# Kernel optimization log

Measured on AMD Instinct MI355X. Metric: run time of the kernel, lower is better.

## Reference

```python
import jax, jax.numpy as jnp
import numpy as np

N_NODES = 100000
N_EDGES = 3200000
ALPHA_KCL = 1.0
ALPHA_KVL = 1.0
EPS = 1e-6


def setup_inputs() -> dict:
    key = jax.random.key(0)
    k1, k2, k3, k4 = jax.random.split(key, 4)
    node_features = jax.random.normal(k1, (N_NODES, 4), dtype=jnp.float32)
    edge_index = jax.random.randint(k2, (2, N_EDGES), 0, N_NODES, dtype=jnp.int64)
    edge_logits = jax.random.normal(k3, (N_EDGES,), dtype=jnp.float32)
    edge_params = jax.random.uniform(k4, (N_EDGES, 2), dtype=jnp.float32)
    return {
        "node_features": node_features,
        "edge_index": edge_index,
        "edge_logits": edge_logits,
        "edge_params": edge_params,
    }


def reference(node_features, edge_index, edge_logits, edge_params):
    n_nodes = node_features.shape[0]
    edge_probs = jax.nn.sigmoid(edge_logits)  # [E]
    src = edge_index[0]  # [E]
    dst = edge_index[1]  # [E]
    v = node_features[:, 0]  # [N] voltage column
    # per-edge current: |v_src - v_dst| / (R + X + eps) * prob
    v_diff = jnp.abs(v[src] - v[dst])
    impedance = edge_params[:, 0] + edge_params[:, 1]
    current = v_diff / (impedance + EPS) * edge_probs  # [E]
    # KCL: each edge subtracts its current at src, adds at dst
    node_sum = (
        jax.ops.segment_sum(current, dst, num_segments=n_nodes)
        - jax.ops.segment_sum(current, src, num_segments=n_nodes)
    )  # [N]
    kcl_loss = jnp.mean(node_sum ** 2)
    # KVL (simplified): mean of per-column unbiased variance of edge_params
    kvl_loss = jnp.var(edge_params, axis=0, ddof=1).mean()
    return ALPHA_KCL * kcl_loss + ALPHA_KVL * kvl_loss
```

## Files before the change

kernel.cpp:

```cpp
#include <hip/hip_runtime.h>
#include <math.h>

#define N_NODES 100000
#define N_EDGES 3200000
#define EPS_F 1e-6f

#define SLICE_N 20000
#define NSLICE  5
#define NCHUNK  64
#define C_PAIRS (N_EDGES / 2 / NCHUNK)
#define SBATCH  8

#define NVARB   6250
#define NKCLB   391

#define PK_OFF    64
#define PART_OFF  (PK_OFF + 2 * N_EDGES)
#define VARP_OFF  (PART_OFF + NCHUNK * N_NODES)
#define KCLP_OFF  (VARP_OFF + 4 * NVARB)
#define WS_FLOATS (KCLP_OFF + NKCLB + 64)

__device__ __forceinline__ float wave_reduce(float v) {
    #pragma unroll
    for (int off = 32; off > 0; off >>= 1) v += __shfl_down(v, off, 64);
    return v;
}

__device__ __forceinline__ void fadd_agent(float* p, float v) {
    unsafeAtomicAdd(p, v);
}

__device__ __forceinline__ unsigned short f2bf(float f) {
    unsigned u = __float_as_uint(f);
    unsigned r = ((u >> 16) & 1u) + 0x7FFFu;
    return (unsigned short)((u + r) >> 16);
}
__device__ __forceinline__ float bf2f(unsigned short h) {
    return __uint_as_float(((unsigned)h) << 16);
}

__global__ __launch_bounds__(256) void prep_kernel(
    const float*  __restrict__ nf,
    const void*   __restrict__ eidx,
    const float*  __restrict__ logits,
    const float2* __restrict__ params,
    float*        __restrict__ ws)
{
    __shared__ float red[4][4];
    const int* i32 = (const int*)eidx;

    int any = 0;
    #pragma unroll
    for (int k = 1; k < 32; k += 2) any |= i32[k];
    const bool is32 = (any != 0);

    const int t = blockIdx.x * blockDim.x + threadIdx.x;

    int2 sp, dp;
    if (is32) {
        sp = ((const int2*)i32)[t];
        dp = ((const int2*)(i32 + N_EDGES))[t];
    } else {
        const int4 a = ((const int4*)i32)[t];
        const int4 b = ((const int4*)(i32 + 2 * N_EDGES))[t];
        sp = make_int2(a.x, a.z);
        dp = make_int2(b.x, b.z);
    }

    const float vs0 = nf[sp.x * 4];
    const float vd0 = nf[dp.x * 4];
    const float vs1 = nf[sp.y * 4];
    const float vd1 = nf[dp.y * 4];

    const float4 pp = ((const float4*)params)[t];
    const float2 lg = ((const float2*)logits)[t];
    const float w0 = (1.0f / (1.0f + __expf(-lg.x))) / (pp.x + pp.y + EPS_F);
    const float w1 = (1.0f / (1.0f + __expf(-lg.y))) / (pp.z + pp.w + EPS_F);
    const float c0 = fabsf(vs0 - vd0) * w0;
    const float c1 = fabsf(vs1 - vd1) * w1;

    int4 pk;
    pk.x = (int)((unsigned)sp.x | ((unsigned)dp.x << 17));
    pk.y = (int)((((unsigned)dp.x) >> 15) | ((unsigned)f2bf(c0) << 2));
    pk.z = (int)((unsigned)sp.y | ((unsigned)dp.y << 17));
    pk.w = (int)((((unsigned)dp.y) >> 15) | ((unsigned)f2bf(c1) << 2));
    ((int4*)(ws + PK_OFF))[t] = pk;

    float s0 = pp.x + pp.z;
    float s1 = pp.y + pp.w;
    float q0 = pp.x * pp.x + pp.z * pp.z;
    float q1 = pp.y * pp.y + pp.w * pp.w;

    s0 = wave_reduce(s0); s1 = wave_reduce(s1);
    q0 = wave_reduce(q0); q1 = wave_reduce(q1);

    const int wid = threadIdx.x >> 6;
    if ((threadIdx.x & 63) == 0) {
        red[wid][0] = s0; red[wid][1] = s1; red[wid][2] = q0; red[wid][3] = q1;
    }
    __syncthreads();
    if (threadIdx.x == 0) {
        float4 o;
        o.x = red[0][0] + red[1][0] + red[2][0] + red[3][0];
        o.y = red[0][1] + red[1][1] + red[2][1] + red[3][1];
        o.z = red[0][2] + red[1][2] + red[2][2] + red[3][2];
        o.w = red[0][3] + red[1][3] + red[2][3] + red[3][3];
        ((float4*)(ws + VARP_OFF))[blockIdx.x] = o;
    }
}

__global__ __launch_bounds__(1024) void scatter_kernel(float* __restrict__ ws)
{
    __shared__ float bins[SLICE_N];

    const int c  = blockIdx.x & (NCHUNK - 1);
    const int s  = blockIdx.x >> 6;
    const unsigned lo = (unsigned)(s * SLICE_N);

    for (int j = threadIdx.x; j < SLICE_N / 4; j += 1024)
        ((float4*)bins)[j] = make_float4(0.f, 0.f, 0.f, 0.f);
    __syncthreads();

    const int4* pk = (const int4*)(ws + PK_OFF);

    const int p0 = c * C_PAIRS;
    const int p1 = p0 + C_PAIRS;

    for (int base = p0 + (int)threadIdx.x; base < p1; base += 1024 * SBATCH) {
        int4 q[SBATCH];
        #pragma unroll
        for (int k = 0; k < SBATCH; ++k) {
            int p = base + k * 1024;
            p = (p < p1) ? p : (p1 - 1);
            q[k] = pk[p];
        }
        #pragma unroll
        for (int k = 0; k < SBATCH; ++k) {
            const int p = base + k * 1024;
            if (p < p1) {
                const unsigned lo0 = (unsigned)q[k].x, hi0 = (unsigned)q[k].y;
                const unsigned lo1 = (unsigned)q[k].z, hi1 = (unsigned)q[k].w;
                const unsigned s0 = (lo0 & 0x1FFFFu) - lo;
                const unsigned d0 = ((lo0 >> 17) | ((hi0 & 3u) << 15)) - lo;
                const unsigned s1 = (lo1 & 0x1FFFFu) - lo;
                const unsigned d1 = ((lo1 >> 17) | ((hi1 & 3u) << 15)) - lo;
                const float c0 = bf2f((unsigned short)((hi0 >> 2) & 0xFFFFu));
                const float c1 = bf2f((unsigned short)((hi1 >> 2) & 0xFFFFu));
                if (d0 < SLICE_N) atomicAdd(&bins[d0],  c0);
                if (s0 < SLICE_N) atomicAdd(&bins[s0], -c0);
                if (d1 < SLICE_N) atomicAdd(&bins[d1],  c1);
                if (s1 < SLICE_N) atomicAdd(&bins[s1], -c1);
            }
        }
    }
    __syncthreads();

    float4* pt4 = (float4*)(ws + PART_OFF + (size_t)c * N_NODES + lo);
    for (int j = threadIdx.x; j < SLICE_N / 4; j += 1024)
        pt4[j] = ((const float4*)bins)[j];
}

__global__ __launch_bounds__(256) void kcl_kernel(float* __restrict__ ws)
{
    __shared__ float red[4];
    const int i = blockIdx.x * blockDim.x + threadIdx.x;
    float acc = 0.f;
    if (i < N_NODES) {
        const float* p = ws + PART_OFF + i;
        float s = 0.f;
        #pragma unroll 8
        for (int c = 0; c < NCHUNK; ++c) s += p[(size_t)c * N_NODES];
        acc = s * s;
    }
    acc = wave_reduce(acc);
    if ((threadIdx.x & 63) == 0) red[threadIdx.x >> 6] = acc;
    __syncthreads();
    if (threadIdx.x == 0)
        ws[KCLP_OFF + blockIdx.x] = red[0] + red[1] + red[2] + red[3];
}

__global__ __launch_bounds__(1024) void final_kernel(
    const float* __restrict__ ws, float* __restrict__ out)
{
    __shared__ float red[16][5];
    float s0 = 0.f, s1 = 0.f, q0 = 0.f, q1 = 0.f, k = 0.f;

    const float4* vp = (const float4*)(ws + VARP_OFF);
    for (int i = threadIdx.x; i < NVARB; i += 1024) {
        const float4 v = vp[i];
        s0 += v.x; s1 += v.y; q0 += v.z; q1 += v.w;
    }
    for (int i = threadIdx.x; i < NKCLB; i += 1024) k += ws[KCLP_OFF + i];

    s0 = wave_reduce(s0); s1 = wave_reduce(s1);
    q0 = wave_reduce(q0); q1 = wave_reduce(q1);
    k  = wave_reduce(k);

    const int wid = threadIdx.x >> 6;
    if ((threadIdx.x & 63) == 0) {
        red[wid][0] = s0; red[wid][1] = s1; red[wid][2] = q0;
        red[wid][3] = q1; red[wid][4] = k;
    }
    __syncthreads();
    if (threadIdx.x == 0) {
        float a0 = 0.f, a1 = 0.f, a2 = 0.f, a3 = 0.f, a4 = 0.f;
        #pragma unroll
        for (int w = 0; w < 16; ++w) {
            a0 += red[w][0]; a1 += red[w][1]; a2 += red[w][2];
            a3 += red[w][3]; a4 += red[w][4];
        }
        const float n    = (float)N_EDGES;
        const float var0 = (a2 - a0 * a0 / n) / (n - 1.0f);
        const float var1 = (a3 - a1 * a1 / n) / (n - 1.0f);
        out[0] = a4 / (float)N_NODES + 0.5f * (var0 + var1);
    }
}

#define FB_NODE_OFF 64
__global__ __launch_bounds__(256) void edge_kernel_fb(
    const float*  __restrict__ nf,
    const void*   __restrict__ eidx,
    const float*  __restrict__ logits,
    const float2* __restrict__ params,
    float*        __restrict__ ws)
{
    const int*       i32 = (const int*)eidx;
    const long long* i64 = (const long long*)eidx;
    int any = 0;
    #pragma unroll
    for (int k = 1; k < 32; k += 2) any |= i32[k];
    const bool is32 = (any != 0);

    float* node_sum = ws + FB_NODE_OFF;
    float* acc      = ws + 1;

    float s0 = 0.f, s1 = 0.f, q0 = 0.f, q1 = 0.f;
    const int tid    = blockIdx.x * blockDim.x + threadIdx.x;
    const int stride = gridDim.x * blockDim.x;
    for (int i = tid; i < N_EDGES; i += stride) {
        int src, dst;
        if (is32) { src = i32[i]; dst = i32[N_EDGES + i]; }
        else      { src = (int)i64[i]; dst = (int)i64[N_EDGES + i]; }
        const float2 ep = params[i];
        const float  p  = 1.0f / (1.0f + __expf(-logits[i]));
        const float cur = fabsf(nf[src * 4] - nf[dst * 4]) / (ep.x + ep.y + EPS_F) * p;
        fadd_agent(node_sum + dst,  cur);
        fadd_agent(node_sum + src, -cur);
        s0 += ep.x; s1 += ep.y; q0 += ep.x * ep.x; q1 += ep.y * ep.y;
    }
    s0 = wave_reduce(s0); s1 = wave_reduce(s1);
    q0 = wave_reduce(q0); q1 = wave_reduce(q1);
    if ((threadIdx.x & 63) == 0) {
        fadd_agent(acc + 0, s0); fadd_agent(acc + 1, s1);
        fadd_agent(acc + 2, q0); fadd_agent(acc + 3, q1);
    }
}

__global__ __launch_bounds__(256) void kcl_kernel_fb(float* __restrict__ ws)
{
    const float* node_sum = ws + FB_NODE_OFF;
    float acc = 0.f;
    const int tid    = blockIdx.x * blockDim.x + threadIdx.x;
    const int stride = gridDim.x * blockDim.x;
    for (int i = tid; i < N_NODES; i += stride) {
        const float v = node_sum[i];
        acc += v * v;
    }
    acc = wave_reduce(acc);
    if ((threadIdx.x & 63) == 0) fadd_agent(ws + 5, acc);
}

__global__ void final_kernel_fb(const float* __restrict__ ws, float* __restrict__ out)
{
    const float s0 = ws[1], s1 = ws[2], q0 = ws[3], q1 = ws[4], k = ws[5];
    const float n  = (float)N_EDGES;
    const float var0 = (q0 - s0 * s0 / n) / (n - 1.0f);
    const float var1 = (q1 - s1 * s1 / n) / (n - 1.0f);
    out[0] = k / (float)N_NODES + 0.5f * (var0 + var1);
}

extern "C" void kernel_launch(void* const* d_in, const int* in_sizes, int n_in,
                              void* d_out, int out_size, void* d_ws, size_t ws_size,
                              hipStream_t stream) {
    const float*  nf     = (const float*)d_in[0];
    const void*   eidx   = d_in[1];
    const float*  logits = (const float*)d_in[2];
    const float2* params = (const float2*)d_in[3];
    float* ws  = (float*)d_ws;
    float* out = (float*)d_out;

    const size_t need = (size_t)WS_FLOATS * sizeof(float);

    if (ws_size >= need) {
        prep_kernel<<<NVARB, 256, 0, stream>>>(nf, eidx, logits, params, ws);
        scatter_kernel<<<NCHUNK * NSLICE, 1024, 0, stream>>>(ws);
        kcl_kernel<<<NKCLB, 256, 0, stream>>>(ws);
        final_kernel<<<1, 1024, 0, stream>>>(ws, out);
    } else {
        hipMemsetAsync(d_ws, 0, 256 + (size_t)N_NODES * sizeof(float), stream);
        edge_kernel_fb<<<2048, 256, 0, stream>>>(nf, eidx, logits, params, ws);
        kcl_kernel_fb<<<200, 256, 0, stream>>>(ws);
        final_kernel_fb<<<1, 1, 0, stream>>>(ws, out);
    }
}
```

Before: 194.8 us.

## Merge final reduction into KCL kernel via last-block counter and retile scatter slices

The separate single-block final kernel is folded into the KCL reduction kernel. A global atomic counter, reset in prep_kernel, identifies the last block to finish, and that block performs the variance and KCL final sums. This removes one kernel launch and its dependency gap. The scatter stage is also retiled to 8 slices of 12500 nodes with 32 chunks, giving smaller LDS bins and fewer partial rows for the KCL kernel to sum. The cost is more passes over the packed edge stream per chunk, plus the added counter and fence logic.

Measured after the change: 186.1 us. 4.5% less time.

```diff
diff --git a/kernel.cpp b/kernel.cpp
--- a/kernel.cpp
+++ b/kernel.cpp
@@ -5,15 +5,16 @@
 #define N_EDGES 3200000
 #define EPS_F 1e-6f
 
-#define SLICE_N 20000
-#define NSLICE  5
-#define NCHUNK  64
+#define SLICE_N 12500
+#define NSLICE  8
+#define NCHUNK  32
 #define C_PAIRS (N_EDGES / 2 / NCHUNK)
 #define SBATCH  8
 
 #define NVARB   6250
 #define NKCLB   391
 
+#define CNT_WORD  32
 #define PK_OFF    64
 #define PART_OFF  (PK_OFF + 2 * N_EDGES)
 #define VARP_OFF  (PART_OFF + NCHUNK * N_NODES)
@@ -55,6 +56,8 @@
     const bool is32 = (any != 0);
 
     const int t = blockIdx.x * blockDim.x + threadIdx.x;
+
+    if (t == 0) ((unsigned*)ws)[CNT_WORD] = 0;
 
     int2 sp, dp;
     if (is32) {
@@ -114,11 +117,10 @@
     __shared__ float bins[SLICE_N];
 
     const int c  = blockIdx.x & (NCHUNK - 1);
-    const int s  = blockIdx.x >> 6;
+    const int s  = blockIdx.x >> 5;
     const unsigned lo = (unsigned)(s * SLICE_N);
 
-    for (int j = threadIdx.x; j < SLICE_N / 4; j += 1024)
-        ((float4*)bins)[j] = make_float4(0.f, 0.f, 0.f, 0.f);
+    for (int j = threadIdx.x; j < SLICE_N; j += 1024) bins[j] = 0.f;
     __syncthreads();
 
     const int4* pk = (const int4*)(ws + PK_OFF);
@@ -160,9 +162,12 @@
         pt4[j] = ((const float4*)bins)[j];
 }
 
-__global__ __launch_bounds__(256) void kcl_kernel(float* __restrict__ ws)
+__global__ __launch_bounds__(256) void kclfinal_kernel(float* __restrict__ ws,
+                                                       float* __restrict__ out)
 {
     __shared__ float red[4];
+    __shared__ unsigned last;
+
     const int i = blockIdx.x * blockDim.x + threadIdx.x;
     float acc = 0.f;
     if (i < N_NODES) {
@@ -175,22 +180,25 @@
     acc = wave_reduce(acc);
     if ((threadIdx.x & 63) == 0) red[threadIdx.x >> 6] = acc;
     __syncthreads();
-    if (threadIdx.x == 0)
+    if (threadIdx.x == 0) {
         ws[KCLP_OFF + blockIdx.x] = red[0] + red[1] + red[2] + red[3];
-}
-
-__global__ __launch_bounds__(1024) void final_kernel(
-    const float* __restrict__ ws, float* __restrict__ out)
-{
-    __shared__ float red[16][5];
+        __threadfence();
+        const unsigned old = atomicAdd((unsigned*)ws + CNT_WORD, 1u);
+        last = (old == NKCLB - 1) ? 1u : 0u;
+    }
+    __syncthreads();
+    if (!last) return;
+
+    __shared__ float red2[4][5];
     float s0 = 0.f, s1 = 0.f, q0 = 0.f, q1 = 0.f, k = 0.f;
 
     const float4* vp = (const float4*)(ws + VARP_OFF);
-    for (int i = threadIdx.x; i < NVARB; i += 1024) {
-        const float4 v = vp[i];
+    for (int j = threadIdx.x; j < NVARB; j += 256) {
+        const float4 v = vp[j];
         s0 += v.x; s1 += v.y; q0 += v.z; q1 += v.w;
     }
-    for (int i = threadIdx.x; i < NKCLB; i += 1024) k += ws[KCLP_OFF + i];
+    for (int j = threadIdx.x; j < NKCLB; j += 256)
+        k += unsafeAtomicAdd(ws + KCLP_OFF + j, 0.0f);
 
     s0 = wave_reduce(s0); s1 = wave_reduce(s1);
     q0 = wave_reduce(q0); q1 = wave_reduce(q1);
@@ -198,16 +206,16 @@
 
     const int wid = threadIdx.x >> 6;
     if ((threadIdx.x & 63) == 0) {
-        red[wid][0] = s0; red[wid][1] = s1; red[wid][2] = q0;
-        red[wid][3] = q1; red[wid][4] = k;
+        red2[wid][0] = s0; red2[wid][1] = s1; red2[wid][2] = q0;
+        red2[wid][3] = q1; red2[wid][4] = k;
     }
     __syncthreads();
     if (threadIdx.x == 0) {
         float a0 = 0.f, a1 = 0.f, a2 = 0.f, a3 = 0.f, a4 = 0.f;
         #pragma unroll
-        for (int w = 0; w < 16; ++w) {
-            a0 += red[w][0]; a1 += red[w][1]; a2 += red[w][2];
-            a3 += red[w][3]; a4 += red[w][4];
+        for (int w = 0; w < 4; ++w) {
+            a0 += red2[w][0]; a1 += red2[w][1]; a2 += red2[w][2];
+            a3 += red2[w][3]; a4 += red2[w][4];
         }
         const float n    = (float)N_EDGES;
         const float var0 = (a2 - a0 * a0 / n) / (n - 1.0f);
@@ -294,8 +302,7 @@
     if (ws_size >= need) {
         prep_kernel<<<NVARB, 256, 0, stream>>>(nf, eidx, logits, params, ws);
         scatter_kernel<<<NCHUNK * NSLICE, 1024, 0, stream>>>(ws);
-        kcl_kernel<<<NKCLB, 256, 0, stream>>>(ws);
-        final_kernel<<<1, 1024, 0, stream>>>(ws, out);
+        kclfinal_kernel<<<NKCLB, 256, 0, stream>>>(ws, out);
     } else {
         hipMemsetAsync(d_ws, 0, 256 + (size_t)N_NODES * sizeof(float), stream);
         edge_kernel_fb<<<2048, 256, 0, stream>>>(nf, eidx, logits, params, ws);
```
